# Performance work log

Measured on AMD Instinct MI355X. Metric: run time of the kernel, lower is better.

The kernel has to match this reference:

```python
import jax, jax.numpy as jnp
import numpy as np

DIM = 2048
HEADS = 16
HEAD_DIM = DIM // HEADS
EPS = 1e-5


def layernorm(x, g, b):
    mu = jnp.mean(x, axis=-1, keepdims=True)
    var = jnp.mean(jnp.square(x - mu), axis=-1, keepdims=True)
    return (x - mu) * jax.lax.rsqrt(var + EPS) * g + b


def bitlinear(x, w):
    # BitNet b1.58: per-tensor ternary weight quant + per-token int8 absmax activation quant
    ws = jnp.clip(jnp.mean(jnp.abs(w)), 1e-5, None)          # weight scale (mean |w|)
    wq = jnp.clip(jnp.round(w / ws), -1.0, 1.0) * ws          # ternary {-1,0,1}*ws
    xs = 127.0 / jnp.clip(jnp.max(jnp.abs(x), axis=-1, keepdims=True), 1e-5, None)
    xq = jnp.clip(jnp.round(x * xs), -128.0, 127.0) / xs      # int8 absmax, dequantized
    return jnp.einsum('bnc,oc->bno', xq, wq)


def attention(x, w_qkv, w_proj):
    B, N, C = x.shape
    qkv = bitlinear(x, w_qkv).reshape(B, N, 3, HEADS, HEAD_DIM)
    q, k, v = [qkv[:, :, i].transpose(0, 2, 1, 3) for i in range(3)]  # [B,H,N,D]
    scores = jnp.einsum('bhqd,bhkd->bhqk', q, k) / jnp.sqrt(jnp.asarray(HEAD_DIM, x.dtype))
    attn = jax.nn.softmax(scores, axis=-1)
    o = jnp.einsum('bhqk,bhkd->bhqd', attn, v)
    o = o.transpose(0, 2, 1, 3).reshape(B, N, C)
    return bitlinear(o, w_proj)


def setup_inputs() -> dict:
    key = jax.random.key(0)
    ks = jax.random.split(key, 9)
    s = 0.02
    return {
        'x': jax.random.normal(ks[0], (2, 2048, DIM), dtype=jnp.float32),
        'w_qkv': jax.random.normal(ks[1], (3 * DIM, DIM), dtype=jnp.float32) * s,
        'w_proj': jax.random.normal(ks[2], (DIM, DIM), dtype=jnp.float32) * s,
        'w_fc1': jax.random.normal(ks[3], (4 * DIM, DIM), dtype=jnp.float32) * s,
        'w_fc2': jax.random.normal(ks[4], (DIM, 4 * DIM), dtype=jnp.float32) * s,
        'g1': jnp.ones((DIM,), jnp.float32),
        'b1': jnp.zeros((DIM,), jnp.float32),
        'g2': jnp.ones((DIM,), jnp.float32),
        'b2': jnp.zeros((DIM,), jnp.float32),
    }


def reference(x, w_qkv, w_proj, w_fc1, w_fc2, g1, b1, g2, b2):
    x = x + attention(layernorm(x, g1, b1), w_qkv, w_proj)
    h = bitlinear(layernorm(x, g2, b2), w_fc1)
    h = jax.nn.gelu(h, approximate=False)
    h = bitlinear(h, w_fc2)
    return x + h
```

## Files before the change

kernel.cpp:

```cpp
#include <hip/hip_runtime.h>
#include <cstdint>

#define DEVI __device__ __forceinline__

typedef int v4i __attribute__((ext_vector_type(4)));
typedef short v8s __attribute__((ext_vector_type(8)));
typedef float v4f __attribute__((ext_vector_type(4)));

DEVI float bf_lo(unsigned u) { return __uint_as_float(u << 16); }
DEVI float bf_hi(unsigned u) { return __uint_as_float(u & 0xffff0000u); }
DEVI float bf2f(unsigned short h) { return __uint_as_float(((unsigned)h) << 16); }
DEVI unsigned short f2bf(float f) {
  unsigned u = __float_as_uint(f);
  u += 0x7fffu + ((u >> 16) & 1u);
  return (unsigned short)(u >> 16);
}

DEVI void async_copy16(void* l, const void* g) {
  __builtin_amdgcn_global_load_lds((const __attribute__((address_space(1))) void*)g,
                                   (__attribute__((address_space(3))) void*)l,
                                   16, 0, 0);
}

DEVI float wave_sum(float v) {
#pragma unroll
  for (int o = 32; o > 0; o >>= 1) v += __shfl_xor(v, o, 64);
  return v;
}
DEVI float wave_max(float v) {
#pragma unroll
  for (int o = 32; o > 0; o >>= 1) v = fmaxf(v, __shfl_xor(v, o, 64));
  return v;
}

__global__ __launch_bounds__(256) void absum_kernel(const float* __restrict__ w, long n,
                                                    float* __restrict__ acc) {
  long stride = (long)gridDim.x * 1024;
  float s = 0.f;
  for (long i = ((long)blockIdx.x * 256 + threadIdx.x) * 4; i < n; i += stride) {
    float4 v = *(const float4*)(w + i);
    s += fabsf(v.x) + fabsf(v.y) + fabsf(v.z) + fabsf(v.w);
  }
  s = wave_sum(s);
  __shared__ float sc[4];
  int tid = threadIdx.x;
  if ((tid & 63) == 0) sc[tid >> 6] = s;
  __syncthreads();
  if (tid == 0) atomicAdd(acc, sc[0] + sc[1] + sc[2] + sc[3]);
}

__global__ __launch_bounds__(256) void wquant_kernel(const float* __restrict__ w, long n4,
                                                     const float* __restrict__ acc, float cnt,
                                                     signed char* __restrict__ out, int kshift) {
  float wsv = fmaxf(acc[0] / cnt, 1e-5f);
  float inv = 1.0f / wsv;
  int K = 1 << kshift;
  long stride = (long)gridDim.x * 256;
  for (long i = (long)blockIdx.x * 256 + threadIdx.x; i < n4; i += stride) {
    float4 v = *(const float4*)(w + i * 4);
    int q0 = max(-1, min(1, (int)rintf(v.x * inv)));
    int q1 = max(-1, min(1, (int)rintf(v.y * inv)));
    int q2 = max(-1, min(1, (int)rintf(v.z * inv)));
    int q3 = max(-1, min(1, (int)rintf(v.w * inv)));
    unsigned r = (q0 & 0xff) | ((q1 & 0xff) << 8) | ((q2 & 0xff) << 16) | ((q3 & 0xff) << 24);
    long flat = i * 4;
    int n = (int)(flat >> kshift);
    int k = (int)(flat & (K - 1));
    long off = ((long)(n >> 4) * (K >> 6) + (k >> 6)) * 1024 +
               (((k >> 4) & 3) * 16 + (n & 15)) * 16 + (k & 15);
    *(unsigned*)(out + off) = r;
  }
}

__global__ __launch_bounds__(256) void ln_quant_kernel(const float* __restrict__ x,
                                                       const float* __restrict__ g,
                                                       const float* __restrict__ b,
                                                       signed char* __restrict__ q,
                                                       float* __restrict__ inv_s) {
  int row = blockIdx.x, tid = threadIdx.x;
  const float4* xr = (const float4*)(x + (long)row * 2048);
  float4 a0 = xr[tid * 2], a1 = xr[tid * 2 + 1];
  float xv[8] = {a0.x, a0.y, a0.z, a0.w, a1.x, a1.y, a1.z, a1.w};
  float s = 0.f, s2 = 0.f;
#pragma unroll
  for (int e = 0; e < 8; ++e) { s += xv[e]; s2 += xv[e] * xv[e]; }
  s = wave_sum(s); s2 = wave_sum(s2);
  __shared__ float sc[8];
  if ((tid & 63) == 0) { sc[tid >> 6] = s; sc[4 + (tid >> 6)] = s2; }
  __syncthreads();
  float mean = (sc[0] + sc[1] + sc[2] + sc[3]) * (1.f / 2048.f);
  float var = (sc[4] + sc[5] + sc[6] + sc[7]) * (1.f / 2048.f) - mean * mean;
  float rs = 1.0f / sqrtf(var + 1e-5f);
  float4 g0 = ((const float4*)g)[tid * 2], g1v = ((const float4*)g)[tid * 2 + 1];
  float4 b0 = ((const float4*)b)[tid * 2], b1v = ((const float4*)b)[tid * 2 + 1];
  float gv[8] = {g0.x, g0.y, g0.z, g0.w, g1v.x, g1v.y, g1v.z, g1v.w};
  float bv[8] = {b0.x, b0.y, b0.z, b0.w, b1v.x, b1v.y, b1v.z, b1v.w};
  float y[8];
  float am = 0.f;
#pragma unroll
  for (int e = 0; e < 8; ++e) {
    y[e] = (xv[e] - mean) * rs * gv[e] + bv[e];
    am = fmaxf(am, fabsf(y[e]));
  }
  am = wave_max(am);
  __syncthreads();
  if ((tid & 63) == 0) sc[tid >> 6] = am;
  __syncthreads();
  am = fmaxf(fmaxf(sc[0], sc[1]), fmaxf(sc[2], sc[3]));
  float c = fmaxf(am, 1e-5f);
  float xs = 127.0f / c;
  union { signed char c8[8]; int2 v; } u;
#pragma unroll
  for (int e = 0; e < 8; ++e) {
    int t = (int)rintf(y[e] * xs);
    u.c8[e] = (signed char)max(-128, min(127, t));
  }
  ((int2*)(q + (long)row * 2048))[tid] = u.v;
  if (tid == 0) inv_s[row] = c * (1.0f / 127.0f);
}

template <int R>
__global__ __launch_bounds__(256) void row_quant_kernel(const unsigned short* __restrict__ in,
                                                        signed char* __restrict__ q,
                                                        float* __restrict__ inv_s) {
  constexpr int V = R / 2048;
  int row = blockIdx.x, tid = threadIdx.x;
  const uint4* p = (const uint4*)(in + (long)row * R);
  float y[V * 8];
  float am = 0.f;
#pragma unroll
  for (int v = 0; v < V; ++v) {
    uint4 d = p[tid * V + v];
    unsigned xw[4] = {d.x, d.y, d.z, d.w};
#pragma unroll
    for (int k = 0; k < 4; ++k) {
      y[v * 8 + k * 2] = bf_lo(xw[k]);
      y[v * 8 + k * 2 + 1] = bf_hi(xw[k]);
    }
  }
#pragma unroll
  for (int e = 0; e < V * 8; ++e) am = fmaxf(am, fabsf(y[e]));
  am = wave_max(am);
  __shared__ float sc[4];
  if ((tid & 63) == 0) sc[tid >> 6] = am;
  __syncthreads();
  am = fmaxf(fmaxf(sc[0], sc[1]), fmaxf(sc[2], sc[3]));
  float c = fmaxf(am, 1e-5f);
  float xs = 127.0f / c;
  signed char* qr = q + (long)row * R;
#pragma unroll
  for (int v = 0; v < V; ++v) {
    union { signed char c8[8]; long l; } u;
#pragma unroll
    for (int k = 0; k < 8; ++k) {
      int t = (int)rintf(y[v * 8 + k] * xs);
      u.c8[k] = (signed char)max(-128, min(127, t));
    }
    ((long*)qr)[tid * V + v] = u.l;
  }
  if (tid == 0) inv_s[row] = c * (1.0f / 127.0f);
}

template <int EPI>
__global__ __launch_bounds__(256)
void gemm_i8(const signed char* __restrict__ A, const signed char* __restrict__ Bp,
             int N, int K, const float* __restrict__ wacc, float wcount,
             const float* __restrict__ inv_s, const float* __restrict__ res,
             void* __restrict__ outp) {
  __shared__ signed char As[2][128 * 128];
  int tid = threadIdx.x;
  int idx = blockIdx.x;
  int r8 = idx & 7, rest = idx >> 3;
  int mb = rest & 31;
  int nb = (rest >> 5) * 8 + r8;
  int m0 = mb * 128, n0 = nb * 128;
  int w = tid >> 6, lane = tid & 63;
  int wm = (w >> 1) * 64, wn = (w & 1) * 64;
  int lr = lane & 15, q = lane >> 4;

  v4i acc[4][4] = {};

  int srow = w * 32 + (lane >> 3);
  int scol = (lane & 7) ^ ((lane >> 3) & 7);
  const signed char* ga = A + (long)(m0 + srow) * K + scol * 16;

  int nkb = K >> 7;
  const signed char* gbp[4];
#pragma unroll
  for (int t = 0; t < 4; ++t) {
    int ntile = (n0 >> 4) + (w & 1) * 4 + t;
    gbp[t] = Bp + (long)ntile * (K >> 6) * 1024 + lane * 16;
  }

  v4i bf_cur[2][4], bf_nxt[2][4];
#pragma unroll
  for (int i = 0; i < 4; ++i)
    async_copy16(&As[0][(w * 256 + i * 64) * 16], ga + i * 8 * K);
#pragma unroll
  for (int s = 0; s < 2; ++s)
#pragma unroll
    for (int t = 0; t < 4; ++t) bf_cur[s][t] = *(const v4i*)(gbp[t] + s * 1024);
  __syncthreads();

  int buf = 0;
  for (int kb = 0; kb < nkb; ++kb) {
    if (kb + 1 < nkb) {
#pragma unroll
      for (int i = 0; i < 4; ++i)
        async_copy16(&As[buf ^ 1][(w * 256 + i * 64) * 16], ga + i * 8 * K + (kb + 1) * 128);
#pragma unroll
      for (int s = 0; s < 2; ++s)
#pragma unroll
        for (int t = 0; t < 4; ++t)
          bf_nxt[s][t] = *(const v4i*)(gbp[t] + ((kb + 1) * 2 + s) * 1024);
    }
#pragma unroll
    for (int s = 0; s < 2; ++s) {
      v4i af[4];
#pragma unroll
      for (int i = 0; i < 4; ++i) {
        int row = wm + i * 16 + lr;
        af[i] = *(const v4i*)(&As[buf][(row * 8 + ((s * 4 + q) ^ (lr & 7))) * 16]);
      }
#pragma unroll
      for (int i = 0; i < 4; ++i)
#pragma unroll
        for (int j = 0; j < 4; ++j)
          acc[i][j] = __builtin_amdgcn_mfma_i32_16x16x64_i8(af[i], bf_cur[s][j], acc[i][j], 0, 0, 0);
    }
    __syncthreads();
    if (kb + 1 < nkb) {
#pragma unroll
      for (int s = 0; s < 2; ++s)
#pragma unroll
        for (int t = 0; t < 4; ++t) bf_cur[s][t] = bf_nxt[s][t];
    }
    buf ^= 1;
  }

  float wsv = fmaxf(wacc[0] / wcount, 1e-5f);
#pragma unroll
  for (int i = 0; i < 4; ++i) {
    int rowbase = m0 + wm + i * 16 + (lane >> 4) * 4;
#pragma unroll
    for (int r = 0; r < 4; ++r) {
      int row = rowbase + r;
      float s = wsv * inv_s[row];
#pragma unroll
      for (int j = 0; j < 4; ++j) {
        int col = n0 + wn + j * 16 + (lane & 15);
        long off = (long)row * N + col;
        float v = (float)acc[i][j][r] * s;
        if constexpr (EPI == 0) {
          ((unsigned short*)outp)[off] = f2bf(v);
        } else if constexpr (EPI == 1) {
          ((float*)outp)[off] = v + res[off];
        } else {
          float gvv = 0.5f * v * (1.0f + erff(v * 0.70710678118654752f));
          ((unsigned short*)outp)[off] = f2bf(gvv);
        }
      }
    }
  }
}


DEVI int sigma_k(int y) {
  return (y & 35) | (((y >> 3) & 1) << 4) | (((y >> 2) & 1) << 3) | (((y >> 4) & 1) << 2);
}

DEVI void stage_k(const unsigned short* kbase_g, int k0, char* ks, int w, int lane) {
#pragma unroll
  for (int i = 0; i < 2; ++i) {
    int c = i * 512 + w * 64 + lane;
    int key = c >> 4;
    int dch = (c & 15) ^ (key & 15);
    async_copy16(ks + (i * 512 + w * 64) * 16,
                 kbase_g + (long)(k0 + sigma_k(key)) * 6144 + dch * 8);
  }
}

DEVI void load_v(const unsigned short* vbase_g, int k0, int kg, int dg, uint2* lv) {
#pragma unroll
  for (int i = 0; i < 4; ++i)
    lv[i] = *(const uint2*)(vbase_g + (long)(k0 + kg * 4 + i) * 6144 + dg * 4);
}

DEVI void repack_v(const uint2* lv, unsigned short* vt, int kg, int dg) {
#pragma unroll
  for (int jd = 0; jd < 4; ++jd) {
    union { unsigned short s[4]; unsigned long long u; } pk;
#pragma unroll
    for (int i = 0; i < 4; ++i) {
      unsigned word = (jd < 2) ? lv[i].x : lv[i].y;
      pk.s[i] = (unsigned short)((jd & 1) ? (word >> 16) : (word & 0xffffu));
    }
    *(unsigned long long*)(vt + (dg * 4 + jd) * 72 + kg * 4) = pk.u;
  }
}

__global__ __launch_bounds__(512, 4)
void fattn_kernel(const unsigned short* __restrict__ qkv, unsigned short* __restrict__ out) {
  constexpr int VROW = 72;
  __shared__ __align__(16) char Ks[2][16384];
  __shared__ __align__(16) unsigned short Vt[2][128 * VROW];

  int tid = threadIdx.x;
  int w = tid >> 6, lane = tid & 63;
  int l = lane & 15, q = lane >> 4;
  int idx = blockIdx.x;
  int r8 = idx & 7, rest = idx >> 3;
  int qt = rest & 15;
  int bh = (rest >> 4) * 8 + r8;
  int bb = bh >> 4, hh = bh & 15;
  const unsigned short* base = qkv + (long)bb * 2048 * 6144;
  int q0 = qt * 128;

  v8s aq[4];
  {
    const unsigned short* qrow = base + (long)(q0 + w * 16 + l) * 6144 + hh * 128;
#pragma unroll
    for (int kf = 0; kf < 4; ++kf) aq[kf] = *(const v8s*)(qrow + kf * 32 + q * 8);
  }

  v4f oacc[8] = {};
  float mrow = -1e30f, lrow = 0.f;

  const unsigned short* kbase_g = base + 2048 + hh * 128;
  const unsigned short* vbase_g = base + 4096 + hh * 128;
  int kg = tid & 15, dg = tid >> 4;
  constexpr float SC = 0.08838834764831845f;

  stage_k(kbase_g, 0, Ks[0], w, lane);
  uint2 lv[4];
  load_v(vbase_g, 0, kg, dg, lv);
  repack_v(lv, Vt[0], kg, dg);
  __syncthreads();

  for (int kt = 0; kt < 32; ++kt) {
    const char* ksc = Ks[kt & 1];
    const unsigned short* vtc = Vt[kt & 1];
    bool more = kt < 31;
    if (more) {
      stage_k(kbase_g, (kt + 1) * 64, Ks[(kt + 1) & 1], w, lane);
      load_v(vbase_g, (kt + 1) * 64, kg, dg, lv);
    }

    v4f sacc[4] = {};
#pragma unroll
    for (int kf = 0; kf < 4; ++kf) {
#pragma unroll
      for (int t = 0; t < 4; ++t) {
        int ch = (t * 16 + l) * 16 + ((kf * 4 + q) ^ l);
        v8s bk = *(const v8s*)(ksc + ch * 16);
        sacc[t] = __builtin_amdgcn_mfma_f32_16x16x32_bf16(bk, aq[kf], sacc[t], 0, 0, 0);
      }
    }

    float rm = -1e30f;
#pragma unroll
    for (int t = 0; t < 4; ++t)
#pragma unroll
      for (int r = 0; r < 4; ++r) rm = fmaxf(rm, sacc[t][r]);
    rm *= SC;
    rm = fmaxf(rm, __shfl_xor(rm, 16, 64));
    rm = fmaxf(rm, __shfl_xor(rm, 32, 64));
    float mnew = fmaxf(mrow, rm);
    if (__any(mnew - mrow > 8.0f)) {
      float alpha = __expf(mrow - mnew);
      mrow = mnew;
      lrow *= alpha;
#pragma unroll
      for (int r = 0; r < 4; ++r) {
        float ao = __shfl(alpha, q * 4 + r, 64);
#pragma unroll
        for (int t = 0; t < 8; ++t) oacc[t][r] *= ao;
      }
    }
    float rs = 0.f;
#pragma unroll
    for (int t = 0; t < 4; ++t)
#pragma unroll
      for (int r = 0; r < 4; ++r) {
        float pv = __expf(fmaf(sacc[t][r], SC, -mrow));
        sacc[t][r] = pv;
        rs += pv;
      }
    rs += __shfl_xor(rs, 16, 64);
    rs += __shfl_xor(rs, 32, 64);
    lrow += rs;

    union { unsigned u[4]; v8s s; } pa[2];
#pragma unroll
    for (int s2 = 0; s2 < 2; ++s2)
#pragma unroll
      for (int j2 = 0; j2 < 4; ++j2) {
        int tt = s2 * 2 + (j2 >> 1);
        int r0 = (j2 & 1) * 2;
        unsigned wrd;
        asm("v_cvt_pk_bf16_f32 %0, %1, %2"
            : "=v"(wrd) : "v"(sacc[tt][r0]), "v"(sacc[tt][r0 + 1]));
        pa[s2].u[j2] = wrd;
      }

#pragma unroll
    for (int s2 = 0; s2 < 2; ++s2) {
#pragma unroll
      for (int t = 0; t < 8; ++t) {
        v8s bv = *(const v8s*)(vtc + (t * 16 + l) * VROW + s2 * 32 + q * 8);
        oacc[t] = __builtin_amdgcn_mfma_f32_16x16x32_bf16(pa[s2].s, bv, oacc[t], 0, 0, 0);
      }
    }

    if (more) repack_v(lv, Vt[(kt + 1) & 1], kg, dg);
    __syncthreads();
  }

#pragma unroll
  for (int r = 0; r < 4; ++r) {
    float lr = __shfl(lrow, q * 4 + r, 64);
    float inv = 1.0f / lr;
    long grow = (long)bb * 2048 + q0 + w * 16 + q * 4 + r;
    unsigned short* orow = out + grow * 2048 + hh * 128;
#pragma unroll
    for (int t = 0; t < 8; ++t) orow[t * 16 + l] = f2bf(oacc[t][r] * inv);
  }
}

extern "C" void kernel_launch(void* const* d_in, const int* in_sizes, int n_in,
                              void* d_out, int out_size, void* d_ws, size_t ws_size,
                              hipStream_t stream) {
  (void)in_sizes; (void)n_in; (void)out_size; (void)ws_size;
  const float* x      = (const float*)d_in[0];
  const float* w_qkv  = (const float*)d_in[1];
  const float* w_proj = (const float*)d_in[2];
  const float* w_fc1  = (const float*)d_in[3];
  const float* w_fc2  = (const float*)d_in[4];
  const float* g1 = (const float*)d_in[5];
  const float* b1 = (const float*)d_in[6];
  const float* g2 = (const float*)d_in[7];
  const float* b2 = (const float*)d_in[8];

  char* wsb = (char*)d_ws;
  float* acc = (float*)wsb;
  size_t off = 256;
  signed char* q8 = (signed char*)(wsb + off);       off += (size_t)4096 * 8192;
  float* invs = (float*)(wsb + off);                 off += 16384;
  signed char* wq_qkv = (signed char*)(wsb + off);   off += (size_t)6144 * 2048;
  signed char* wq_proj = (signed char*)(wsb + off);  off += (size_t)2048 * 2048;
  signed char* wq_fc1 = (signed char*)(wsb + off);   off += (size_t)8192 * 2048;
  signed char* wq_fc2 = (signed char*)(wsb + off);   off += (size_t)2048 * 8192;
  unsigned short* qkvh = (unsigned short*)(wsb + off); off += (size_t)4096 * 8192 * 2;
  unsigned short* obuf = (unsigned short*)(wsb + off); off += (size_t)4096 * 2048 * 2;
  float* x2 = (float*)(wsb + off);                   off += (size_t)4096 * 2048 * 4;

  hipMemsetAsync(acc, 0, 256, stream);

  absum_kernel<<<dim3(1024), 256, 0, stream>>>(w_qkv, (long)6144 * 2048, acc + 0);
  absum_kernel<<<dim3(512),  256, 0, stream>>>(w_proj, (long)2048 * 2048, acc + 1);
  absum_kernel<<<dim3(1024), 256, 0, stream>>>(w_fc1, (long)8192 * 2048, acc + 2);
  absum_kernel<<<dim3(1024), 256, 0, stream>>>(w_fc2, (long)2048 * 8192, acc + 3);

  wquant_kernel<<<dim3(1024), 256, 0, stream>>>(w_qkv, (long)6144 * 2048 / 4, acc + 0, 12582912.f, wq_qkv, 11);
  wquant_kernel<<<dim3(1024), 256, 0, stream>>>(w_proj, (long)2048 * 2048 / 4, acc + 1, 4194304.f, wq_proj, 11);
  wquant_kernel<<<dim3(1024), 256, 0, stream>>>(w_fc1, (long)8192 * 2048 / 4, acc + 2, 16777216.f, wq_fc1, 11);
  wquant_kernel<<<dim3(1024), 256, 0, stream>>>(w_fc2, (long)2048 * 8192 / 4, acc + 3, 16777216.f, wq_fc2, 13);

  ln_quant_kernel<<<4096, 256, 0, stream>>>(x, g1, b1, q8, invs);
  gemm_i8<0><<<48 * 32, 256, 0, stream>>>(q8, wq_qkv, 6144, 2048, acc + 0, 12582912.f, invs, nullptr, qkvh);
  fattn_kernel<<<512, 512, 0, stream>>>(qkvh, obuf);
  row_quant_kernel<2048><<<4096, 256, 0, stream>>>(obuf, q8, invs);
  gemm_i8<1><<<16 * 32, 256, 0, stream>>>(q8, wq_proj, 2048, 2048, acc + 1, 4194304.f, invs, x, x2);
  ln_quant_kernel<<<4096, 256, 0, stream>>>(x2, g2, b2, q8, invs);
  gemm_i8<2><<<64 * 32, 256, 0, stream>>>(q8, wq_fc1, 8192, 2048, acc + 2, 16777216.f, invs, nullptr, qkvh);
  row_quant_kernel<8192><<<4096, 256, 0, stream>>>(qkvh, q8, invs);
  gemm_i8<1><<<16 * 32, 256, 0, stream>>>(q8, wq_fc2, 2048, 8192, acc + 3, 16777216.f, invs, x2, (float*)d_out);
}
```

Measured before the change: 761.1 us.

## Add 256x256-tile int8 GEMM with register-prefetched B for QKV and FC1

Adds a new int8 MFMA GEMM kernel that uses 256x256 output tiles with 512 threads. A is double-buffered in LDS through async global-to-LDS copies, and B fragments are prefetched straight into registers one k-step ahead. Barriers, explicit waitcnt and setprio are placed by hand to overlap the loads with MFMA work. The QKV and FC1 projections switch to this kernel to get more data reuse per tile and less global/LDS traffic. In exchange, register pressure rises with 128 accumulator registers per lane, and the grid has fewer, larger blocks, which may underfill the CUs on the QKV shape.

```diff
diff --git a/kernel.cpp b/kernel.cpp
--- a/kernel.cpp
+++ b/kernel.cpp
@@ -264,6 +264,151 @@
   }
 }
 
+#define GIB_PHASE(RB, BFC, VMISSUE, WAITSTR, TAIL)                                      \
+  {                                                                                     \
+    v4i af[4];                                                                          \
+    _Pragma("unroll") for (int j = 0; j < 4; ++j) {                                     \
+      int m = 2 * p + (j >> 1), kc = j & 1;                                             \
+      int row = wm + m * 16 + lr;                                                       \
+      af[j] = *(const v4i*)(&As[(RB)][(row * 8 + ((kc * 4 + q) ^ (lr & 7))) * 16]);     \
+    }                                                                                   \
+    __builtin_amdgcn_sched_barrier(0);                                                  \
+    VMISSUE                                                                             \
+    __builtin_amdgcn_sched_barrier(0);                                                  \
+    __builtin_amdgcn_s_barrier();                                                       \
+    asm volatile(WAITSTR ::: "memory");                                                 \
+    __builtin_amdgcn_sched_barrier(0);                                                  \
+    __builtin_amdgcn_s_setprio(1);                                                      \
+    _Pragma("unroll") for (int j = 0; j < 2; ++j)                                       \
+      _Pragma("unroll") for (int t = 0; t < 4; ++t)                                     \
+        _Pragma("unroll") for (int kc = 0; kc < 2; ++kc)                                \
+          acc[2 * p + j][t] = __builtin_amdgcn_mfma_i32_16x16x64_i8(                    \
+              af[j * 2 + kc], BFC[kc][t], acc[2 * p + j][t], 0, 0, 0);                  \
+    __builtin_amdgcn_s_setprio(0);                                                      \
+    __builtin_amdgcn_sched_barrier(0);                                                  \
+    TAIL                                                                                \
+    __builtin_amdgcn_s_barrier();                                                       \
+  }
+
+#define GIB_STAGE(RBD)                                                                  \
+  _Pragma("unroll") for (int i = 0; i < 4; ++i)                                         \
+    async_copy16(&As[(RBD)][(w * 256 + i * 64) * 16],                                   \
+                 ga + (long)i * 8 * K + (kb + 1) * 128);
+
+#define GIB_LOADB(DST, HALF)                                                            \
+  _Pragma("unroll") for (int t = 0; t < 4; ++t)                                         \
+    asm volatile("global_load_dwordx4 %0, %1, off"                                      \
+                 : "=v"(DST[HALF][t])                                                   \
+                 : "v"(gbp[t] + (long)((kb + 1) * 2 + (HALF)) * 1024)                   \
+                 : "memory");
+
+#define GIB_VMTAIL                                                                      \
+  asm volatile("s_waitcnt vmcnt(8)" ::: "memory");                                      \
+  __builtin_amdgcn_sched_barrier(0);
+
+#define GIB_ITER_MAIN(RB, BFC, BFN)                                                     \
+  {                                                                                     \
+    { constexpr int p = 0;                                                              \
+      GIB_PHASE(RB, BFC, GIB_STAGE((RB) ^ 1), "s_waitcnt vmcnt(4) lgkmcnt(0)", ) }      \
+    { constexpr int p = 1;                                                              \
+      GIB_PHASE(RB, BFC, GIB_LOADB(BFN, 0), "s_waitcnt lgkmcnt(0)", ) }                 \
+    { constexpr int p = 2;                                                              \
+      GIB_PHASE(RB, BFC, GIB_LOADB(BFN, 1), "s_waitcnt lgkmcnt(0)", ) }                 \
+    { constexpr int p = 3;                                                              \
+      GIB_PHASE(RB, BFC, , "s_waitcnt lgkmcnt(0)", GIB_VMTAIL) }                        \
+  }
+
+#define GIB_ITER_LAST(RB, BFC)                                                          \
+  {                                                                                     \
+    { constexpr int p = 0;                                                              \
+      GIB_PHASE(RB, BFC, , "s_waitcnt vmcnt(0) lgkmcnt(0)", ) }                         \
+    { constexpr int p = 1;                                                              \
+      GIB_PHASE(RB, BFC, , "s_waitcnt lgkmcnt(0)", ) }                                  \
+    { constexpr int p = 2;                                                              \
+      GIB_PHASE(RB, BFC, , "s_waitcnt lgkmcnt(0)", ) }                                  \
+    { constexpr int p = 3;                                                              \
+      GIB_PHASE(RB, BFC, , "s_waitcnt lgkmcnt(0)", ) }                                  \
+  }
+
+template <int EPI>
+__global__ __launch_bounds__(512, 2)
+void gemm_i8_big(const signed char* __restrict__ A, const signed char* __restrict__ Bp,
+                 int N, int K, const float* __restrict__ wacc, float wcount,
+                 const float* __restrict__ inv_s, const float* __restrict__ res,
+                 void* __restrict__ outp) {
+  __shared__ signed char As[2][256 * 128];
+  int tid = threadIdx.x;
+  int idx = blockIdx.x;
+  int r8 = idx & 7, rest = idx >> 3;
+  int mb = rest & 15;
+  int nb = (rest >> 4) * 8 + r8;
+  int m0 = mb * 256, n0 = nb * 256;
+  int w = tid >> 6, lane = tid & 63;
+  int wm = (w >> 2) * 128, wn = (w & 3) * 64;
+  int lr = lane & 15, q = lane >> 4;
+
+  v4i acc[8][4] = {};
+
+  int srow = w * 32 + (lane >> 3);
+  int scol = (lane & 7) ^ ((lane >> 3) & 7);
+  const signed char* ga = A + (long)(m0 + srow) * K + scol * 16;
+
+  int nkt = K >> 7;
+  const signed char* gbp[4];
+#pragma unroll
+  for (int t = 0; t < 4; ++t) {
+    int ntile = ((n0 + wn) >> 4) + t;
+    gbp[t] = Bp + (long)ntile * (K >> 6) * 1024 + lane * 16;
+  }
+
+  v4i bfA[2][4], bfB[2][4];
+#pragma unroll
+  for (int i = 0; i < 4; ++i)
+    async_copy16(&As[0][(w * 256 + i * 64) * 16], ga + (long)i * 8 * K);
+  __builtin_amdgcn_sched_barrier(0);
+#pragma unroll
+  for (int s = 0; s < 2; ++s)
+#pragma unroll
+    for (int t = 0; t < 4; ++t)
+      asm volatile("global_load_dwordx4 %0, %1, off"
+                   : "=v"(bfA[s][t]) : "v"(gbp[t] + (long)s * 1024) : "memory");
+  __builtin_amdgcn_sched_barrier(0);
+  asm volatile("s_waitcnt vmcnt(8)" ::: "memory");
+  __builtin_amdgcn_sched_barrier(0);
+  __builtin_amdgcn_s_barrier();
+
+  for (int kb2 = 0; kb2 < nkt - 2; kb2 += 2) {
+    { int kb = kb2;     GIB_ITER_MAIN(0, bfA, bfB) }
+    { int kb = kb2 + 1; GIB_ITER_MAIN(1, bfB, bfA) }
+  }
+  { int kb = nkt - 2; GIB_ITER_MAIN(0, bfA, bfB) }
+  GIB_ITER_LAST(1, bfB)
+
+  float wsv = fmaxf(wacc[0] / wcount, 1e-5f);
+#pragma unroll
+  for (int m = 0; m < 8; ++m) {
+    int rowbase = m0 + wm + m * 16 + q * 4;
+#pragma unroll
+    for (int r = 0; r < 4; ++r) {
+      int row = rowbase + r;
+      float s = wsv * inv_s[row];
+#pragma unroll
+      for (int j = 0; j < 4; ++j) {
+        int col = n0 + wn + j * 16 + lr;
+        long off = (long)row * N + col;
+        float v = (float)acc[m][j][r] * s;
+        if constexpr (EPI == 0) {
+          ((unsigned short*)outp)[off] = f2bf(v);
+        } else if constexpr (EPI == 1) {
+          ((float*)outp)[off] = v + res[off];
+        } else {
+          float gvv = 0.5f * v * (1.0f + erff(v * 0.70710678118654752f));
+          ((unsigned short*)outp)[off] = f2bf(gvv);
+        }
+      }
+    }
+  }
+}
 
 DEVI int sigma_k(int y) {
   return (y & 35) | (((y >> 3) & 1) << 4) | (((y >> 2) & 1) << 3) | (((y >> 4) & 1) << 2);
@@ -467,12 +612,12 @@
   wquant_kernel<<<dim3(1024), 256, 0, stream>>>(w_fc2, (long)2048 * 8192 / 4, acc + 3, 16777216.f, wq_fc2, 13);
 
   ln_quant_kernel<<<4096, 256, 0, stream>>>(x, g1, b1, q8, invs);
-  gemm_i8<0><<<48 * 32, 256, 0, stream>>>(q8, wq_qkv, 6144, 2048, acc + 0, 12582912.f, invs, nullptr, qkvh);
+  gemm_i8_big<0><<<16 * 24, 512, 0, stream>>>(q8, wq_qkv, 6144, 2048, acc + 0, 12582912.f, invs, nullptr, qkvh);
   fattn_kernel<<<512, 512, 0, stream>>>(qkvh, obuf);
   row_quant_kernel<2048><<<4096, 256, 0, stream>>>(obuf, q8, invs);
   gemm_i8<1><<<16 * 32, 256, 0, stream>>>(q8, wq_proj, 2048, 2048, acc + 1, 4194304.f, invs, x, x2);
   ln_quant_kernel<<<4096, 256, 0, stream>>>(x2, g2, b2, q8, invs);
-  gemm_i8<2><<<64 * 32, 256, 0, stream>>>(q8, wq_fc1, 8192, 2048, acc + 2, 16777216.f, invs, nullptr, qkvh);
+  gemm_i8_big<2><<<16 * 32, 512, 0, stream>>>(q8, wq_fc1, 8192, 2048, acc + 2, 16777216.f, invs, nullptr, qkvh);
   row_quant_kernel<8192><<<4096, 256, 0, stream>>>(qkvh, q8, invs);
   gemm_i8<1><<<16 * 32, 256, 0, stream>>>(q8, wq_fc2, 2048, 8192, acc + 3, 16777216.f, invs, x2, (float*)d_out);
 }
```

After: 766.1 us. Within noise of the previous version (+0.7%).
